# Optimization experiments

Measured on AMD Instinct MI355X. Metric: run time of the kernel, lower is better.

The kernel has to match this reference:

```python
import jax, jax.numpy as jnp
import numpy as np

DIM = 2048
K_DIM = 2048
Q_HEADS = 16
KV_HEADS = 4
HEAD_DIM = DIM // Q_HEADS  # 128
KV_DIM = HEAD_DIM * KV_HEADS  # 512
MAX_LEN = 2048
ROPE_THETA = 10000.0
ROPE_FACTOR = 8.0


def _rope_cos_sin(seq_len):
    # Faithful to generate_sin_cos_pos_emb with is_causal=True
    d = HEAD_DIM
    seq_eff = max(seq_len, MAX_LEN)
    base_adj = (ROPE_FACTOR * seq_eff / MAX_LEN - (ROPE_FACTOR - 1.0)) ** (d / (d - 2))
    adjusted_base = ROPE_THETA * base_adj
    inv_freq = 1.0 / adjusted_base ** (np.arange(0, d, 2, dtype=np.float32) / d)
    pos = np.arange(seq_len, dtype=np.float32)  # causal: no centering
    freqs = pos[:, None] * inv_freq[None, :]            # [S, d/2]
    emb = np.concatenate([freqs, freqs], axis=-1)        # [S, d]
    return jnp.asarray(np.cos(emb), jnp.float32), jnp.asarray(np.sin(emb), jnp.float32)


def _rotate_half(x):
    x1, x2 = jnp.split(x, 2, axis=-1)
    return jnp.concatenate([-x2, x1], axis=-1)


def setup_inputs() -> dict:
    key = jax.random.key(0)
    ks = jax.random.split(key, 12)
    B, S = 1, 2048
    s_in = 1.0 / np.sqrt(DIM)
    s_k = 1.0 / np.sqrt(K_DIM)
    return {
        "query": jax.random.normal(ks[0], (B, S, DIM), jnp.float32),
        "key": jax.random.normal(ks[1], (B, S, K_DIM), jnp.float32),
        "value": jax.random.normal(ks[2], (B, S, K_DIM), jnp.float32),
        "Wq": jax.random.uniform(ks[3], (DIM, DIM), jnp.float32, -s_in, s_in),
        "bq": jax.random.uniform(ks[4], (DIM,), jnp.float32, -s_in, s_in),
        "Wk": jax.random.uniform(ks[5], (KV_DIM, K_DIM), jnp.float32, -s_k, s_k),
        "bk": jax.random.uniform(ks[6], (KV_DIM,), jnp.float32, -s_k, s_k),
        "Wv": jax.random.uniform(ks[7], (KV_DIM, K_DIM), jnp.float32, -s_k, s_k),
        "bv": jax.random.uniform(ks[8], (KV_DIM,), jnp.float32, -s_k, s_k),
        "Wo": jax.random.uniform(ks[9], (DIM, DIM), jnp.float32, -s_in, s_in),
        "bo": jax.random.uniform(ks[10], (DIM,), jnp.float32, -s_in, s_in),
    }


def reference(query, key, value, Wq, bq, Wk, bk, Wv, bv, Wo, bo):
    B, S, _ = query.shape
    scale = HEAD_DIM ** -0.5

    q = query @ Wq.T + bq                                   # [B,S,DIM]
    k = key @ Wk.T + bk                                     # [B,S,KV_DIM]
    v = value @ Wv.T + bv                                   # [B,S,KV_DIM]

    q = q.reshape(B, S, Q_HEADS, HEAD_DIM)
    k = k.reshape(B, S, KV_HEADS, HEAD_DIM)
    v = v.reshape(B, S, KV_HEADS, HEAD_DIM)

    cos, sin = _rope_cos_sin(S)                              # [S,D]
    cos = cos[None, :, None, :]
    sin = sin[None, :, None, :]
    q = q * cos + _rotate_half(q) * sin
    k = k * cos + _rotate_half(k) * sin

    # [B,H,S,D]
    q = q.transpose(0, 2, 1, 3)
    k = k.transpose(0, 2, 1, 3)
    v = v.transpose(0, 2, 1, 3)

    rep = Q_HEADS // KV_HEADS
    k = jnp.repeat(k, rep, axis=1)
    v = jnp.repeat(v, rep, axis=1)

    scores = jnp.einsum('bhqd,bhkd->bhqk', q, k) * scale
    causal = jnp.tril(jnp.ones((S, S), bool))
    scores = jnp.where(causal[None, None], scores, jnp.finfo(scores.dtype).min)
    attn = jax.nn.softmax(scores, axis=-1)
    out = jnp.einsum('bhqk,bhkd->bhqd', attn, v)             # [B,H,S,D]

    out = out.transpose(0, 2, 1, 3).reshape(B, S, DIM)
    return out @ Wo.T + bo
```

## Files before the change

kernel.cpp:

```cpp
#include <hip/hip_runtime.h>
#include <stdint.h>

typedef __attribute__((ext_vector_type(8))) short short8;
typedef __attribute__((ext_vector_type(4))) float f32x4;
typedef __attribute__((ext_vector_type(4))) unsigned short u16x4;
typedef unsigned short bf16_t;

__device__ __forceinline__ bf16_t f2bf(float f) {
  union { float f; uint32_t u; } x; x.f = f;
  uint32_t r = x.u + 0x7fffu + ((x.u >> 16) & 1u);
  return (bf16_t)(r >> 16);
}

__device__ __forceinline__ void ld_g2l_16(const bf16_t* g, bf16_t* l) {
  __builtin_amdgcn_global_load_lds(
      (const __attribute__((address_space(1))) void*)g,
      (__attribute__((address_space(3))) void*)l, 16, 0, 0);
}

__global__ void rope_tab(float* __restrict__ CS, float* __restrict__ SN) {
  int idx = blockIdx.x * 256 + threadIdx.x;
  int i = idx & 63, pos = idx >> 6;
  float ang = (float)pos * exp2f((float)i * -0.2076205059f);
  CS[idx] = cosf(ang);
  SN[idx] = sinf(ang);
}

__global__ void convert_all(const float* __restrict__ s0, const float* __restrict__ s1,
                            const float* __restrict__ s2, const float* __restrict__ s3,
                            const float* __restrict__ s4, const float* __restrict__ s5,
                            const float* __restrict__ s6,
                            bf16_t* __restrict__ d0, bf16_t* __restrict__ d1,
                            bf16_t* __restrict__ d2, bf16_t* __restrict__ d3,
                            bf16_t* __restrict__ d4, bf16_t* __restrict__ d5,
                            bf16_t* __restrict__ d6) {
  int i = blockIdx.x * 256 + threadIdx.x;
  const float* src; bf16_t* dst; int off;
  if (i < 5 * 1048576) {
    int t = i >> 20; off = i & 1048575;
    if (t == 0)      { src = s0; dst = d0; }
    else if (t == 1) { src = s1; dst = d1; }
    else if (t == 2) { src = s2; dst = d2; }
    else if (t == 3) { src = s3; dst = d3; }
    else             { src = s4; dst = d4; }
  } else {
    int j = i - 5 * 1048576;
    if (j < 262144) { src = s5; dst = d5; off = j; }
    else            { src = s6; dst = d6; off = j - 262144; }
  }
  f32x4 v = *(const f32x4*)(src + (size_t)off * 4);
  u16x4 o;
  o[0] = f2bf(v[0]); o[1] = f2bf(v[1]); o[2] = f2bf(v[2]); o[3] = f2bf(v[3]);
  *(u16x4*)(dst + (size_t)off * 4) = o;
}

template <int MODE>
__device__ __forceinline__ void gemm_core(
    bf16_t* __restrict__ As, bf16_t* __restrict__ Bs,
    const bf16_t* __restrict__ A, const bf16_t* __restrict__ Bm,
    const float* __restrict__ bias, void* __restrict__ Cout,
    int N, int K, int m0, int n0,
    const float* __restrict__ CS, const float* __restrict__ SN) {
  const int tid = threadIdx.x;
  const int lane = tid & 63, quad = lane >> 4, l16 = lane & 15;
  const int wv = tid >> 6;
  const int m_off = wv * 32;
  const int c0 = tid, c1 = tid + 256;
  const int r0 = c0 >> 2, col0 = (c0 & 3) * 8;
  const int r1 = c1 >> 2, col1 = (c1 & 3) * 8;

  f32x4 acc[2][8];
  const f32x4 zf = {0.f, 0.f, 0.f, 0.f};
#pragma unroll
  for (int mi = 0; mi < 2; ++mi)
#pragma unroll
    for (int ni = 0; ni < 8; ++ni) acc[mi][ni] = zf;

  const bf16_t* Ap0 = A + (size_t)(m0 + r0) * K + col0;
  const bf16_t* Ap1 = A + (size_t)(m0 + r1) * K + col1;
  const bf16_t* Bp0 = Bm + (size_t)(n0 + r0) * K + col0;
  const bf16_t* Bp1 = Bm + (size_t)(n0 + r1) * K + col1;
  bf16_t* lA0 = As + c0 * 8;  bf16_t* lA1 = As + c1 * 8;
  bf16_t* lB0 = Bs + c0 * 8;  bf16_t* lB1 = Bs + c1 * 8;

  for (int k0 = 0; k0 < K; k0 += 32) {
    ld_g2l_16(Ap0 + k0, lA0);
    ld_g2l_16(Ap1 + k0, lA1);
    ld_g2l_16(Bp0 + k0, lB0);
    ld_g2l_16(Bp1 + k0, lB1);
    __syncthreads();
    short8 af[2], bf[8];
#pragma unroll
    for (int mi = 0; mi < 2; ++mi)
      af[mi] = *(const short8*)(&As[(m_off + mi * 16 + l16) * 32 + quad * 8]);
#pragma unroll
    for (int ni = 0; ni < 8; ++ni)
      bf[ni] = *(const short8*)(&Bs[(ni * 16 + l16) * 32 + quad * 8]);
#pragma unroll
    for (int mi = 0; mi < 2; ++mi)
#pragma unroll
      for (int ni = 0; ni < 8; ++ni)
        acc[mi][ni] = __builtin_amdgcn_mfma_f32_16x16x32_bf16(
            af[mi], bf[ni], acc[mi][ni], 0, 0, 0);
    __syncthreads();
  }

  if (MODE == 0 || MODE == 2) {
#pragma unroll
    for (int mi = 0; mi < 2; ++mi)
#pragma unroll
      for (int ni = 0; ni < 8; ++ni) {
        int n = n0 + ni * 16 + l16;
        int mbase = m0 + m_off + mi * 16 + quad * 4;
        float bv = bias[n];
#pragma unroll
        for (int r = 0; r < 4; ++r) {
          float v = acc[mi][ni][r] + bv;
          int m = mbase + r;
          if (MODE == 0) ((float*)Cout)[(size_t)m * N + n] = v;
          else           ((bf16_t*)Cout)[(size_t)n * 2048 + m] = f2bf(v);
        }
      }
  } else {
    const float scale = (MODE == 3) ? 0.08838834764831845f : 1.0f;
    bf16_t* dst = (bf16_t*)Cout;
#pragma unroll
    for (int mi = 0; mi < 2; ++mi)
#pragma unroll
      for (int r = 0; r < 4; ++r) {
        int m = m0 + m_off + mi * 16 + quad * 4 + r;
#pragma unroll
        for (int ni = 0; ni < 4; ++ni) {
          int i = ni * 16 + l16;
          int n_lo = n0 + i;
          float v1 = acc[mi][ni][r] + bias[n_lo];
          float v2 = acc[mi][ni + 4][r] + bias[n_lo + 64];
          float c = CS[m * 64 + i];
          float s = SN[m * 64 + i];
          float o1 = (v1 * c - v2 * s) * scale;
          float o2 = (v2 * c + v1 * s) * scale;
          dst[(size_t)m * N + n_lo] = f2bf(o1);
          dst[(size_t)m * N + n_lo + 64] = f2bf(o2);
        }
      }
  }
}

__global__ __launch_bounds__(256) void gemm_qkv(
    const bf16_t* __restrict__ qb, const bf16_t* __restrict__ kb,
    const bf16_t* __restrict__ vb, const bf16_t* __restrict__ wqb,
    const bf16_t* __restrict__ wkb, const bf16_t* __restrict__ wvb,
    const float* __restrict__ bq, const float* __restrict__ bk,
    const float* __restrict__ bv, bf16_t* __restrict__ Qr,
    bf16_t* __restrict__ Kr, bf16_t* __restrict__ Vt,
    const float* __restrict__ CS, const float* __restrict__ SN) {
  __shared__ __align__(16) bf16_t As[128 * 32];
  __shared__ __align__(16) bf16_t Bs[128 * 32];
  int bx = blockIdx.x, m0 = blockIdx.y * 128;
  if (bx < 16)
    gemm_core<3>(As, Bs, qb, wqb, bq, Qr, 2048, 2048, m0, bx * 128, CS, SN);
  else if (bx < 20)
    gemm_core<4>(As, Bs, kb, wkb, bk, Kr, 512, 2048, m0, (bx - 16) * 128, CS, SN);
  else
    gemm_core<2>(As, Bs, vb, wvb, bv, Vt, 512, 2048, m0, (bx - 20) * 128, CS, SN);
}

__global__ __launch_bounds__(256) void gemm_o(
    const bf16_t* __restrict__ Ob, const bf16_t* __restrict__ wob,
    const float* __restrict__ bo, float* __restrict__ out) {
  __shared__ __align__(16) bf16_t As[128 * 32];
  __shared__ __align__(16) bf16_t Bs[128 * 32];
  gemm_core<0>(As, Bs, Ob, wob, bo, out, 2048, 2048,
               blockIdx.y * 128, blockIdx.x * 128, nullptr, nullptr);
}

__global__ __launch_bounds__(256, 4) void attn_fwd(
    const bf16_t* __restrict__ Qr, const bf16_t* __restrict__ Kr,
    const bf16_t* __restrict__ Vt, float* __restrict__ Op0,
    float* __restrict__ Op1, float* __restrict__ Lp0,
    float* __restrict__ Lp1) {
  const int h = blockIdx.y;
  const int bx = blockIdx.x;
  const int qt = 31 - (bx >> 1);
  const int ch = bx & 1;
  const int T = qt + 1, sp = (T + 1) >> 1;
  const int t_beg = ch ? sp : 0;
  const int t_end = ch ? T : sp;
  float* __restrict__ Op = ch ? Op1 : Op0;
  float* __restrict__ Lp = ch ? Lp1 : Lp0;

  const int tid = threadIdx.x;
  const int wv = tid >> 6, lane = tid & 63, quad = lane >> 4, l16 = lane & 15;
  const int q_base = qt * 64 + wv * 16;
  const int hkv = h >> 2;
  const int qg = q_base + l16;

  __shared__ __align__(16) bf16_t Ks[64 * 136];
  __shared__ __align__(16) bf16_t Vs[128 * 72];

  short8 qf[4];
  {
    const bf16_t* qp = Qr + (size_t)qg * 2048 + h * 128 + quad * 8;
#pragma unroll
    for (int kc = 0; kc < 4; ++kc) qf[kc] = *(const short8*)(qp + kc * 32);
  }

  const f32x4 zf = {0.f, 0.f, 0.f, 0.f};
  f32x4 o[8];
#pragma unroll
  for (int di = 0; di < 8; ++di) o[di] = zf;
  float l_acc = 0.f;

  for (int t = t_beg; t < t_end; ++t) {
    const int k0 = t * 64;
#pragma unroll
    for (int j = 0; j < 4; ++j) {
      int cid = tid + j * 256;
      int row = cid >> 4, c = cid & 15;
      f32x4 tmp = *(const f32x4*)(&Kr[(size_t)(k0 + row) * 512 + hkv * 128 + c * 8]);
      *(f32x4*)(&Ks[row * 136 + c * 8]) = tmp;
    }
#pragma unroll
    for (int j = 0; j < 4; ++j) {
      int cid = tid + j * 256;
      int row = cid >> 3, c = cid & 7;
      f32x4 tmp = *(const f32x4*)(&Vt[(size_t)(hkv * 128 + row) * 2048 + k0 + c * 8]);
      *(f32x4*)(&Vs[row * 72 + c * 8]) = tmp;
    }
    __syncthreads();

    f32x4 sacc[4];
#pragma unroll
    for (int sub = 0; sub < 4; ++sub) sacc[sub] = zf;
#pragma unroll
    for (int sub = 0; sub < 4; ++sub)
#pragma unroll
      for (int kc = 0; kc < 4; ++kc) {
        short8 kf = *(const short8*)(&Ks[(sub * 16 + l16) * 136 + kc * 32 + quad * 8]);
        sacc[sub] = __builtin_amdgcn_mfma_f32_16x16x32_bf16(kf, qf[kc], sacc[sub], 0, 0, 0);
      }

    const bool diag = (k0 + 63 > q_base);
    uint32_t Dw[4][2];
#pragma unroll
    for (int sub = 0; sub < 4; ++sub) {
      float pv[4];
#pragma unroll
      for (int r = 0; r < 4; ++r) {
        float e = __expf(sacc[sub][r]);
        if (diag) {
          int kg = k0 + sub * 16 + quad * 4 + r;
          if (kg > qg) e = 0.f;
        }
        pv[r] = e;
        l_acc += e;
      }
      Dw[sub][0] = (uint32_t)f2bf(pv[0]) | ((uint32_t)f2bf(pv[1]) << 16);
      Dw[sub][1] = (uint32_t)f2bf(pv[2]) | ((uint32_t)f2bf(pv[3]) << 16);
    }

    const int aA = ((((quad * 2) & 3) << 4) + l16) << 2;
    const int aB = ((((quad * 2 + 1) & 3) << 4) + l16) << 2;
    const bool losel = quad < 2;
#define BPERM(a, x) ((uint32_t)__builtin_amdgcn_ds_bpermute((a), (int)(x)))
    union { uint32_t w[4]; short8 v; } U0, U1;
    {
      uint32_t t0, t1;
      t0 = BPERM(aA, Dw[0][0]); t1 = BPERM(aA, Dw[1][0]); U0.w[0] = losel ? t0 : t1;
      t0 = BPERM(aA, Dw[0][1]); t1 = BPERM(aA, Dw[1][1]); U0.w[1] = losel ? t0 : t1;
      t0 = BPERM(aB, Dw[0][0]); t1 = BPERM(aB, Dw[1][0]); U0.w[2] = losel ? t0 : t1;
      t0 = BPERM(aB, Dw[0][1]); t1 = BPERM(aB, Dw[1][1]); U0.w[3] = losel ? t0 : t1;
      t0 = BPERM(aA, Dw[2][0]); t1 = BPERM(aA, Dw[3][0]); U1.w[0] = losel ? t0 : t1;
      t0 = BPERM(aA, Dw[2][1]); t1 = BPERM(aA, Dw[3][1]); U1.w[1] = losel ? t0 : t1;
      t0 = BPERM(aB, Dw[2][0]); t1 = BPERM(aB, Dw[3][0]); U1.w[2] = losel ? t0 : t1;
      t0 = BPERM(aB, Dw[2][1]); t1 = BPERM(aB, Dw[3][1]); U1.w[3] = losel ? t0 : t1;
    }
#undef BPERM
    const short8 pf0 = U0.v, pf1 = U1.v;

#pragma unroll
    for (int di = 0; di < 8; ++di) {
      short8 vf0 = *(const short8*)(&Vs[(di * 16 + l16) * 72 + quad * 8]);
      short8 vf1 = *(const short8*)(&Vs[(di * 16 + l16) * 72 + 32 + quad * 8]);
      o[di] = __builtin_amdgcn_mfma_f32_16x16x32_bf16(pf0, vf0, o[di], 0, 0, 0);
      o[di] = __builtin_amdgcn_mfma_f32_16x16x32_bf16(pf1, vf1, o[di], 0, 0, 0);
    }
    __syncthreads();
  }

  float lf = l_acc;
  lf += __shfl_xor(lf, 16);
  lf += __shfl_xor(lf, 32);
  if (quad == 0) Lp[(h << 11) + q_base + l16] = lf;
#pragma unroll
  for (int di = 0; di < 8; ++di)
#pragma unroll
    for (int r = 0; r < 4; ++r) {
      size_t row = q_base + quad * 4 + r;
      size_t col = h * 128 + di * 16 + l16;
      Op[row * 2048 + col] = o[di][r];
    }
}

__global__ __launch_bounds__(256) void attn_combine(
    const float* __restrict__ Op0, const float* __restrict__ Op1,
    const float* __restrict__ Lp0, const float* __restrict__ Lp1,
    bf16_t* __restrict__ Ob) {
  int idx = blockIdx.x * 256 + threadIdx.x;
  size_t base = (size_t)idx * 8;
  int row = (int)(base >> 11);
  int col = (int)(base & 2047);
  int h = col >> 7;
  float li = 1.0f / (Lp0[(h << 11) + row] + Lp1[(h << 11) + row]);
  f32x4 a0 = *(const f32x4*)(Op0 + base);
  f32x4 a1 = *(const f32x4*)(Op0 + base + 4);
  f32x4 b0 = *(const f32x4*)(Op1 + base);
  f32x4 b1 = *(const f32x4*)(Op1 + base + 4);
  u16x4 o0, o1;
#pragma unroll
  for (int j = 0; j < 4; ++j) {
    o0[j] = f2bf((a0[j] + b0[j]) * li);
    o1[j] = f2bf((a1[j] + b1[j]) * li);
  }
  *(u16x4*)(Ob + base) = o0;
  *(u16x4*)(Ob + base + 4) = o1;
}

extern "C" void kernel_launch(void* const* d_in, const int* in_sizes, int n_in,
                              void* d_out, int out_size, void* d_ws, size_t ws_size,
                              hipStream_t stream) {
  (void)in_sizes; (void)n_in; (void)out_size; (void)ws_size;
  const float* query = (const float*)d_in[0];
  const float* key = (const float*)d_in[1];
  const float* value = (const float*)d_in[2];
  const float* Wq = (const float*)d_in[3];
  const float* bq = (const float*)d_in[4];
  const float* Wk = (const float*)d_in[5];
  const float* bk = (const float*)d_in[6];
  const float* Wv = (const float*)d_in[7];
  const float* bv = (const float*)d_in[8];
  const float* Wo = (const float*)d_in[9];
  const float* bo = (const float*)d_in[10];
  float* out = (float*)d_out;

  char* ws = (char*)d_ws;
  const size_t MB = 1024 * 1024;
  bf16_t* qb  = (bf16_t*)(ws + 0 * MB);
  bf16_t* kb  = (bf16_t*)(ws + 8 * MB);
  bf16_t* vb  = (bf16_t*)(ws + 16 * MB);
  bf16_t* wqb = (bf16_t*)(ws + 24 * MB);
  bf16_t* wkb = (bf16_t*)(ws + 32 * MB);
  bf16_t* wvb = (bf16_t*)(ws + 34 * MB);
  bf16_t* wob = (bf16_t*)(ws + 36 * MB);
  bf16_t* Qr  = (bf16_t*)(ws + 44 * MB);
  bf16_t* Kr  = (bf16_t*)(ws + 52 * MB);
  bf16_t* Vt  = (bf16_t*)(ws + 54 * MB);
  bf16_t* Ob  = (bf16_t*)(ws + 56 * MB);
  float*  CS  = (float*)(ws + 64 * MB);
  float*  SN  = (float*)(ws + 64 * MB + 512 * 1024);

  float* Op0 = (float*)(ws + 0 * MB);
  float* Op1 = (float*)(ws + 16 * MB);
  float* Lp0 = (float*)(ws + 32 * MB);
  float* Lp1 = (float*)(ws + 32 * MB + 256 * 1024);

  rope_tab<<<512, 256, 0, stream>>>(CS, SN);
  convert_all<<<22528, 256, 0, stream>>>(query, key, value, Wq, Wo, Wk, Wv,
                                         qb, kb, vb, wqb, wob, wkb, wvb);
  gemm_qkv<<<dim3(24, 16), 256, 0, stream>>>(qb, kb, vb, wqb, wkb, wvb,
                                             bq, bk, bv, Qr, Kr, Vt, CS, SN);
  attn_fwd<<<dim3(64, 16), 256, 0, stream>>>(Qr, Kr, Vt, Op0, Op1, Lp0, Lp1);
  attn_combine<<<2048, 256, 0, stream>>>(Op0, Op1, Lp0, Lp1, Ob);
  gemm_o<<<dim3(16, 16), 256, 0, stream>>>(Ob, wob, bo, out);
}
```

Measured before the change: 318.3 us.

## Double-buffer attention K/V tiles with async LDS loads and drop split-KV combine

The attention kernel now stages K and V tiles into double-buffered, XOR-swizzled shared memory using global_load_lds, so the next tile's loads overlap the current tile's MFMA work. The two-way split over key tiles and the separate combine kernel are removed: each block processes a full query tile and writes normalized bf16 output directly, with heads ordered so half the grid runs long tiles first and half short tiles first. This removes the fp32 partial-output round trip and one kernel launch, but halves the number of blocks and doubles LDS usage, lowering occupancy (launch bounds changed to 2) and possibly worsening load balance.

```diff
diff --git a/kernel.cpp b/kernel.cpp
--- a/kernel.cpp
+++ b/kernel.cpp
@@ -174,29 +174,23 @@
                blockIdx.y * 128, blockIdx.x * 128, nullptr, nullptr);
 }
 
-__global__ __launch_bounds__(256, 4) void attn_fwd(
+__global__ __launch_bounds__(256, 2) void attn_fwd(
     const bf16_t* __restrict__ Qr, const bf16_t* __restrict__ Kr,
-    const bf16_t* __restrict__ Vt, float* __restrict__ Op0,
-    float* __restrict__ Op1, float* __restrict__ Lp0,
-    float* __restrict__ Lp1) {
+    const bf16_t* __restrict__ Vt, bf16_t* __restrict__ Oo) {
   const int h = blockIdx.y;
   const int bx = blockIdx.x;
-  const int qt = 31 - (bx >> 1);
-  const int ch = bx & 1;
-  const int T = qt + 1, sp = (T + 1) >> 1;
-  const int t_beg = ch ? sp : 0;
-  const int t_end = ch ? T : sp;
-  float* __restrict__ Op = ch ? Op1 : Op0;
-  float* __restrict__ Lp = ch ? Lp1 : Lp0;
+  const int qt = (h < 8) ? (31 - bx) : bx;
+  const int T = qt + 1;
 
   const int tid = threadIdx.x;
   const int wv = tid >> 6, lane = tid & 63, quad = lane >> 4, l16 = lane & 15;
   const int q_base = qt * 64 + wv * 16;
   const int hkv = h >> 2;
   const int qg = q_base + l16;
-
-  __shared__ __align__(16) bf16_t Ks[64 * 136];
-  __shared__ __align__(16) bf16_t Vs[128 * 72];
+  const int swzE = (l16 & 7) << 3;
+
+  __shared__ __align__(16) bf16_t Ks[2][64 * 128];
+  __shared__ __align__(16) bf16_t Vs[2][128 * 64];
 
   short8 qf[4];
   {
@@ -211,23 +205,32 @@
   for (int di = 0; di < 8; ++di) o[di] = zf;
   float l_acc = 0.f;
 
-  for (int t = t_beg; t < t_end; ++t) {
+  auto STAGE = [&](int buf, int t) {
     const int k0 = t * 64;
-#pragma unroll
-    for (int j = 0; j < 4; ++j) {
-      int cid = tid + j * 256;
-      int row = cid >> 4, c = cid & 15;
-      f32x4 tmp = *(const f32x4*)(&Kr[(size_t)(k0 + row) * 512 + hkv * 128 + c * 8]);
-      *(f32x4*)(&Ks[row * 136 + c * 8]) = tmp;
-    }
-#pragma unroll
-    for (int j = 0; j < 4; ++j) {
-      int cid = tid + j * 256;
-      int row = cid >> 3, c = cid & 7;
-      f32x4 tmp = *(const f32x4*)(&Vt[(size_t)(hkv * 128 + row) * 2048 + k0 + c * 8]);
-      *(f32x4*)(&Vs[row * 72 + c * 8]) = tmp;
-    }
-    __syncthreads();
+    bf16_t* KB = &Ks[buf][0];
+    bf16_t* VB = &Vs[buf][0];
+#pragma unroll
+    for (int m = 0; m < 4; ++m) {
+      int rK = wv * 16 + m * 4 + (lane >> 4);
+      const bf16_t* gK = Kr + (size_t)(k0 + rK) * 512 + hkv * 128
+                         + (((lane & 15) ^ ((4 * (m & 1)) | quad)) << 3);
+      ld_g2l_16(gK, KB + rK * 128 + ((lane & 15) << 3));
+      int rV = wv * 32 + m * 8 + (lane >> 3);
+      const bf16_t* gV = Vt + (size_t)(hkv * 128 + rV) * 2048 + k0
+                         + (((lane & 7) ^ ((lane >> 3) & 7)) << 3);
+      ld_g2l_16(gV, VB + rV * 64 + ((lane & 7) << 3));
+    }
+  };
+
+  STAGE(0, 0);
+  __syncthreads();
+  int buf = 0;
+
+  for (int t = 0; t < T; ++t) {
+    if (t + 1 < T) STAGE(buf ^ 1, t + 1);
+    const bf16_t* KB = &Ks[buf][0];
+    const bf16_t* VB = &Vs[buf][0];
+    const int k0 = t * 64;
 
     f32x4 sacc[4];
 #pragma unroll
@@ -236,7 +239,8 @@
     for (int sub = 0; sub < 4; ++sub)
 #pragma unroll
       for (int kc = 0; kc < 4; ++kc) {
-        short8 kf = *(const short8*)(&Ks[(sub * 16 + l16) * 136 + kc * 32 + quad * 8]);
+        short8 kf = *(const short8*)(
+            &KB[(sub * 16 + l16) * 128 + ((kc * 32 + quad * 8) ^ swzE)]);
         sacc[sub] = __builtin_amdgcn_mfma_f32_16x16x32_bf16(kf, qf[kc], sacc[sub], 0, 0, 0);
       }
 
@@ -280,50 +284,33 @@
 
 #pragma unroll
     for (int di = 0; di < 8; ++di) {
-      short8 vf0 = *(const short8*)(&Vs[(di * 16 + l16) * 72 + quad * 8]);
-      short8 vf1 = *(const short8*)(&Vs[(di * 16 + l16) * 72 + 32 + quad * 8]);
+      short8 vf0 = *(const short8*)(
+          &VB[(di * 16 + l16) * 64 + ((quad * 8) ^ swzE)]);
+      short8 vf1 = *(const short8*)(
+          &VB[(di * 16 + l16) * 64 + ((quad * 8 + 32) ^ swzE)]);
       o[di] = __builtin_amdgcn_mfma_f32_16x16x32_bf16(pf0, vf0, o[di], 0, 0, 0);
       o[di] = __builtin_amdgcn_mfma_f32_16x16x32_bf16(pf1, vf1, o[di], 0, 0, 0);
     }
+
+    __asm__ volatile("s_waitcnt vmcnt(0)" ::: "memory");
     __syncthreads();
+    buf ^= 1;
   }
 
   float lf = l_acc;
   lf += __shfl_xor(lf, 16);
   lf += __shfl_xor(lf, 32);
-  if (quad == 0) Lp[(h << 11) + q_base + l16] = lf;
+  float linv[4];
+#pragma unroll
+  for (int r = 0; r < 4; ++r) linv[r] = 1.0f / __shfl(lf, quad * 4 + r, 64);
 #pragma unroll
   for (int di = 0; di < 8; ++di)
 #pragma unroll
     for (int r = 0; r < 4; ++r) {
       size_t row = q_base + quad * 4 + r;
       size_t col = h * 128 + di * 16 + l16;
-      Op[row * 2048 + col] = o[di][r];
-    }
-}
-
-__global__ __launch_bounds__(256) void attn_combine(
-    const float* __restrict__ Op0, const float* __restrict__ Op1,
-    const float* __restrict__ Lp0, const float* __restrict__ Lp1,
-    bf16_t* __restrict__ Ob) {
-  int idx = blockIdx.x * 256 + threadIdx.x;
-  size_t base = (size_t)idx * 8;
-  int row = (int)(base >> 11);
-  int col = (int)(base & 2047);
-  int h = col >> 7;
-  float li = 1.0f / (Lp0[(h << 11) + row] + Lp1[(h << 11) + row]);
-  f32x4 a0 = *(const f32x4*)(Op0 + base);
-  f32x4 a1 = *(const f32x4*)(Op0 + base + 4);
-  f32x4 b0 = *(const f32x4*)(Op1 + base);
-  f32x4 b1 = *(const f32x4*)(Op1 + base + 4);
-  u16x4 o0, o1;
-#pragma unroll
-  for (int j = 0; j < 4; ++j) {
-    o0[j] = f2bf((a0[j] + b0[j]) * li);
-    o1[j] = f2bf((a1[j] + b1[j]) * li);
-  }
-  *(u16x4*)(Ob + base) = o0;
-  *(u16x4*)(Ob + base + 4) = o1;
+      Oo[row * 2048 + col] = f2bf(o[di][r] * linv[r]);
+    }
 }
 
 extern "C" void kernel_launch(void* const* d_in, const int* in_sizes, int n_in,
@@ -359,17 +346,11 @@
   float*  CS  = (float*)(ws + 64 * MB);
   float*  SN  = (float*)(ws + 64 * MB + 512 * 1024);
 
-  float* Op0 = (float*)(ws + 0 * MB);
-  float* Op1 = (float*)(ws + 16 * MB);
-  float* Lp0 = (float*)(ws + 32 * MB);
-  float* Lp1 = (float*)(ws + 32 * MB + 256 * 1024);
-
   rope_tab<<<512, 256, 0, stream>>>(CS, SN);
   convert_all<<<22528, 256, 0, stream>>>(query, key, value, Wq, Wo, Wk, Wv,
                                          qb, kb, vb, wqb, wob, wkb, wvb);
   gemm_qkv<<<dim3(24, 16), 256, 0, stream>>>(qb, kb, vb, wqb, wkb, wvb,
                                              bq, bk, bv, Qr, Kr, Vt, CS, SN);
-  attn_fwd<<<dim3(64, 16), 256, 0, stream>>>(Qr, Kr, Vt, Op0, Op1, Lp0, Lp1);
-  attn_combine<<<2048, 256, 0, stream>>>(Op0, Op1, Lp0, Lp1, Ob);
+  attn_fwd<<<dim3(32, 16), 256, 0, stream>>>(Qr, Kr, Vt, Ob);
   gemm_o<<<dim3(16, 16), 256, 0, stream>>>(Ob, wob, bo, out);
 }
```

Result: faster. 289.2 us (-9.1%).
